# Kernel optimization log

Measured on AMD Instinct MI355X. Metric: run time of the kernel, lower is better.

Reference implementation:

```python
import jax, jax.numpy as jnp
import numpy as np

D_MODEL = 768
N_HEADS = 12
HEAD_DIM = D_MODEL // N_HEADS


def setup_inputs() -> dict:
    key = jax.random.key(0)
    k_x, k_wqkv, k_bqkv, k_wo, k_bo = jax.random.split(key, 5)
    s = 1.0 / np.sqrt(D_MODEL)
    return {
        "x": jax.random.normal(k_x, (4, 2048, D_MODEL), dtype=jnp.float32),
        "W_qkv": jax.random.uniform(k_wqkv, (D_MODEL, 3 * D_MODEL), jnp.float32, -s, s),
        "b_qkv": jax.random.uniform(k_bqkv, (3 * D_MODEL,), jnp.float32, -s, s),
        "W_out": jax.random.uniform(k_wo, (D_MODEL, D_MODEL), jnp.float32, -s, s),
        "b_out": jax.random.uniform(k_bo, (D_MODEL,), jnp.float32, -s, s),
    }


def reference(x, W_qkv, b_qkv, W_out, b_out):
    B, S, D = x.shape
    qkv = x @ W_qkv + b_qkv  # [B, S, 3D]
    q, k, v = jnp.split(qkv, 3, axis=-1)

    def heads(t):
        return t.reshape(B, S, N_HEADS, HEAD_DIM).transpose(0, 2, 1, 3)  # [B,H,S,Dh]

    q, k, v = heads(q), heads(k), heads(v)
    scale = HEAD_DIM ** -0.5
    scores = jnp.einsum("bhqd,bhkd->bhqk", q, k) * scale  # [B,H,S,S]
    causal = jnp.tril(jnp.ones((S, S), dtype=bool))
    scores = jnp.where(causal, scores, -jnp.inf)
    probs = jax.nn.softmax(scores, axis=-1)
    out = jnp.einsum("bhqk,bhkd->bhqd", probs, v)  # [B,H,S,Dh]
    out = out.transpose(0, 2, 1, 3).reshape(B, S, D)
    return out @ W_out + b_out
```

## Files before the change

### kernel.cpp

```cpp
#include <hip/hip_runtime.h>
#include <hip/hip_bf16.h>

#define D_MODEL 768
#define NH 12
#define HD 64
#define BATCH 4
#define SEQ 2048
#define BHN (BATCH*NH)
#define MROWS (BATCH*SEQ)

typedef unsigned short u16;
typedef unsigned int u32;
typedef __attribute__((ext_vector_type(8))) short short8;
typedef __attribute__((ext_vector_type(4))) float f32x4;

__device__ inline u16 f2bf(float f){
  union { __hip_bfloat16 h; u16 u; } cv; cv.h = __float2bfloat16(f); return cv.u;
}
__device__ inline u32 pack_bf2(float a, float b){
  return (u32)f2bf(a) | ((u32)f2bf(b) << 16);
}

__device__ inline void async_copy16(const void* g, void* l){
  __builtin_amdgcn_global_load_lds(
      (const __attribute__((address_space(1))) void*)g,
      (__attribute__((address_space(3))) void*)l, 16, 0, 0);
}

__global__ void cast4_kernel(const float* __restrict__ in, u16* __restrict__ out, int n4){
  int i = blockIdx.x*blockDim.x + threadIdx.x;
  if (i < n4){
    const float4 v = ((const float4*)in)[i];
    ushort4 o;
    o.x = f2bf(v.x); o.y = f2bf(v.y); o.z = f2bf(v.z); o.w = f2bf(v.w);
    ((ushort4*)out)[i] = o;
  }
}

__global__ void transpose_cast_kernel(const float* __restrict__ w, u16* __restrict__ wt,
                                      int K, int N){
  __shared__ u16 tile[64][65];
  int k0 = blockIdx.x*64, n0 = blockIdx.y*64;
  int c = threadIdx.x & 63, r0 = threadIdx.x >> 6;
  #pragma unroll
  for (int r = r0; r < 64; r += 4)
    tile[c][r] = f2bf(w[(size_t)(k0+r)*N + n0 + c]);
  __syncthreads();
  #pragma unroll
  for (int r = r0; r < 64; r += 4)
    wt[(size_t)(n0+r)*K + k0 + c] = tile[r][c];
}

template<int EPI>
__launch_bounds__(256)
__global__ void gemm_bf16(const u16* __restrict__ A, const u16* __restrict__ Bt,
                          const float* __restrict__ bias, float* __restrict__ outf,
                          u16* __restrict__ oq, u16* __restrict__ ok, u16* __restrict__ ovt,
                          int M, int N, int K)
{
  __shared__ alignas(16) char smem[49152];
  const int tid = threadIdx.x, wave = tid>>6, lane = tid&63;
  const int lr = lane&15, lg = lane>>4;
  const int m0 = blockIdx.x*128, n0 = blockIdx.y*128;
  const int wr = (wave>>1)*64, wc = (wave&1)*64;
  f32x4 acc[4][4] = {};
  const int srow = wave*32 + (lane>>2);
  const int schk = (lane&3) ^ ((lane>>3)&3);
  const int fo   = ((lg ^ ((lr>>1)&3)) << 4);

  auto stage = [&](int kt, int buf){
    char* Ab = smem + buf*16384;
    char* Bb = Ab + 8192;
    #pragma unroll
    for (int i = 0; i < 2; i++){
      int r = srow + i*16;
      async_copy16(A  + (size_t)(m0 + r)*K + kt + schk*8, Ab + (wave*32 + i*16)*64);
      async_copy16(Bt + (size_t)(n0 + r)*K + kt + schk*8, Bb + (wave*32 + i*16)*64);
    }
  };

  const int NT = K >> 5;
  stage(0, 0);
  if (NT > 1) stage(32, 1);
  int c = 0, sb = 2;
  for (int t = 0; t < NT; t++){
    if (t+1 < NT) asm volatile("s_waitcnt vmcnt(4)" ::: "memory");
    else          asm volatile("s_waitcnt vmcnt(0)" ::: "memory");
    __builtin_amdgcn_s_barrier();
    if (t+2 < NT){
      stage((t+2)<<5, sb);
      sb = (sb==2) ? 0 : sb+1;
    }

    const char* Ac = smem + c*16384;
    const char* Bc = Ac + 8192;
    c = (c==2) ? 0 : c+1;
    short8 a[4], b[4];
    #pragma unroll
    for (int mi = 0; mi < 4; mi++)
      a[mi] = *(const short8*)(Ac + (wr + mi*16 + lr)*64 + fo);
    #pragma unroll
    for (int ni = 0; ni < 4; ni++)
      b[ni] = *(const short8*)(Bc + (wc + ni*16 + lr)*64 + fo);
    #pragma unroll
    for (int mi = 0; mi < 4; mi++)
      #pragma unroll
      for (int ni = 0; ni < 4; ni++)
        acc[mi][ni] = __builtin_amdgcn_mfma_f32_16x16x32_bf16(a[mi], b[ni], acc[mi][ni], 0, 0, 0);
  }

  #pragma unroll
  for (int mi = 0; mi < 4; mi++)
  #pragma unroll
  for (int ni = 0; ni < 4; ni++)
  #pragma unroll
  for (int j = 0; j < 4; j++){
    int m = m0 + wr + mi*16 + lg*4 + j;
    int n = n0 + wc + ni*16 + lr;
    float v = acc[mi][ni][j] + bias[n];
    if (EPI == 0){
      outf[(size_t)m*N + n] = v;
    } else {
      int b_ = m >> 11, s = m & 2047;
      int t  = (n >= 1536) ? 2 : (n >= 768 ? 1 : 0);
      int hn = n - t*768;
      int h = hn >> 6, d = hn & 63;
      size_t base = (size_t)(b_*NH + h);
      if (t == 0)      oq [(base*SEQ + s)*HD + d] = f2bf(v * 0.1803368801f);
      else if (t == 1) ok [(base*SEQ + s)*HD + d] = f2bf(v);
      else             ovt[(base*HD + d)*SEQ + s] = f2bf(v);
    }
  }
}

__launch_bounds__(256, 3)
__global__ void attn_kernel(const u16* __restrict__ q, const u16* __restrict__ k,
                            const u16* __restrict__ vt, u16* __restrict__ aout)
{
  __shared__ alignas(16) char smem[53248];

  const int b1 = blockIdx.x;
  const int xcd = b1 & 7, grp = b1 >> 3;
  const int bh = xcd*6 + (grp >> 4);
  const int p  = grp & 15;
  const int hi = 31 - p;
  const int tid = threadIdx.x, wave = tid>>6, lane = tid&63;
  const int lr = lane&15, lg = lane>>4;
  const int b_ = bh / NH, h_ = bh % NH;
  const u16* qp = q  + (size_t)bh*SEQ*HD;
  const u16* kp = k  + (size_t)bh*SEQ*HD;
  const u16* vp = vt + (size_t)bh*HD*SEQ;
  char* Pw = smem + 32768 + wave*5120;
  const int fswz = (lr&7)<<4;
  const int c8s = (lane&7) ^ (lane>>3);
  const int nkv = hi + 1;

  auto stageKV = [&](int kv0, int buf){
    char* Kb = smem + buf*16384;
    char* Vb = Kb + 8192;
    #pragma unroll
    for (int r = 0; r < 2; r++){
      int row = wave*16 + r*8 + (lane>>3);
      async_copy16(kp + (size_t)(kv0 + row)*HD + c8s*8, Kb + (wave*16 + r*8)*128);
      async_copy16(vp + (size_t)row*SEQ + kv0 + c8s*8,  Vb + (wave*16 + r*8)*128);
    }
  };

  const int qrow[2] = { hi*64 + wave*16 + lr, p*64 + wave*16 + lr };

  short8 bq[2][2];
  #pragma unroll
  for (int h = 0; h < 2; h++)
    #pragma unroll
    for (int ks = 0; ks < 2; ks++)
      bq[h][ks] = *(const short8*)(qp + (size_t)qrow[h]*HD + ks*32 + lg*8);

  float mrow[2] = {-INFINITY, -INFINITY};
  float lsum[2] = {0.f, 0.f};
  f32x4 o[4][2] = {};

  stageKV(0, 0);

  auto softmax_pack = [&](f32x4 (&s)[4][2], int h, bool domask, int kv0, int qr){
    if (domask){
      #pragma unroll
      for (int ni = 0; ni < 4; ni++)
        #pragma unroll
        for (int jj = 0; jj < 4; jj++){
          int col = kv0 + ni*16 + lg*4 + jj;
          if (col > qr) s[ni][h][jj] = -1e30f;
        }
    }
    float v0 = fmaxf(fmaxf(s[0][h][0], s[0][h][1]), fmaxf(s[0][h][2], s[0][h][3]));
    float v1 = fmaxf(fmaxf(s[1][h][0], s[1][h][1]), fmaxf(s[1][h][2], s[1][h][3]));
    float v2 = fmaxf(fmaxf(s[2][h][0], s[2][h][1]), fmaxf(s[2][h][2], s[2][h][3]));
    float v3 = fmaxf(fmaxf(s[3][h][0], s[3][h][1]), fmaxf(s[3][h][2], s[3][h][3]));
    float vloc = fmaxf(fmaxf(v0, v1), fmaxf(v2, v3));
    if (!__all(vloc - mrow[h] <= 8.0f)){
      float v = fmaxf(vloc, __shfl_xor(vloc, 16));
      v = fmaxf(v, __shfl_xor(v, 32));
      float mn = fmaxf(mrow[h], v);
      float alpha = __builtin_amdgcn_exp2f(mrow[h] - mn);
      mrow[h] = mn;
      lsum[h] *= alpha;
      #pragma unroll
      for (int ni = 0; ni < 4; ni++)
        #pragma unroll
        for (int jj = 0; jj < 4; jj++)
          o[ni][h][jj] *= alpha;
    }
    const float mn = mrow[h];
    char* hb = Pw + h*2560;
    float psum = 0.f;
    #pragma unroll
    for (int ni = 0; ni < 4; ni++){
      float p0 = __builtin_amdgcn_exp2f(s[ni][h][0] - mn);
      float p1 = __builtin_amdgcn_exp2f(s[ni][h][1] - mn);
      float p2 = __builtin_amdgcn_exp2f(s[ni][h][2] - mn);
      float p3 = __builtin_amdgcn_exp2f(s[ni][h][3] - mn);
      psum += (p0+p1) + (p2+p3);
      int tl = lr + 16*(((ni&1)<<1) | (lg>>1));
      int wb = ((ni>>1)<<2) | ((lg&1)<<1);
      *(u32*)(hb + tl*40 + wb*4)     = pack_bf2(p0, p1);
      *(u32*)(hb + tl*40 + wb*4 + 4) = pack_bf2(p2, p3);
    }
    lsum[h] += psum;
  };

  auto read_pb = [&](int h, short8& r0, short8& r1){
    const char* hb = Pw + h*2560 + (size_t)lane*40;
    union { u32 w[4]; short8 v; } a, b;
    a.w[0] = *(const u32*)(hb);      a.w[1] = *(const u32*)(hb + 4);
    a.w[2] = *(const u32*)(hb + 8);  a.w[3] = *(const u32*)(hb + 12);
    b.w[0] = *(const u32*)(hb + 16); b.w[1] = *(const u32*)(hb + 20);
    b.w[2] = *(const u32*)(hb + 24); b.w[3] = *(const u32*)(hb + 28);
    r0 = a.v; r1 = b.v;
  };

  int kvb = 0;

  #pragma unroll 1
  for (; kvb <= p; kvb++){
    const int c = kvb & 1;
    const int kv0 = kvb*64;
    asm volatile("s_waitcnt vmcnt(0)" ::: "memory");
    __builtin_amdgcn_s_barrier();
    if (kvb+1 < nkv) stageKV(kv0 + 64, c^1);

    const char* Kb = smem + c*16384;
    const char* Vb = Kb + 8192;

    f32x4 s[4][2] = {};
    __builtin_amdgcn_s_setprio(1);
    #pragma unroll
    for (int ni = 0; ni < 4; ni++){
      short8 k0 = *(const short8*)(Kb + (ni*16+lr)*128 + ((lg*16) ^ fswz));
      short8 k1 = *(const short8*)(Kb + (ni*16+lr)*128 + ((64 + lg*16) ^ fswz));
      #pragma unroll
      for (int h = 0; h < 2; h++){
        s[ni][h] = __builtin_amdgcn_mfma_f32_16x16x32_bf16(k0, bq[h][0], s[ni][h], 0,0,0);
        s[ni][h] = __builtin_amdgcn_mfma_f32_16x16x32_bf16(k1, bq[h][1], s[ni][h], 0,0,0);
      }
    }
    __builtin_amdgcn_s_setprio(0);

    softmax_pack(s, 0, false, kv0, qrow[0]);
    softmax_pack(s, 1, kvb == p, kv0, qrow[1]);

    short8 pb[2][2];
    read_pb(0, pb[0][0], pb[0][1]);
    read_pb(1, pb[1][0], pb[1][1]);

    __builtin_amdgcn_s_setprio(1);
    #pragma unroll
    for (int ni = 0; ni < 4; ni++){
      short8 v0 = *(const short8*)(Vb + (ni*16+lr)*128 + ((lg*16) ^ fswz));
      short8 v1 = *(const short8*)(Vb + (ni*16+lr)*128 + ((64 + lg*16) ^ fswz));
      #pragma unroll
      for (int h = 0; h < 2; h++){
        o[ni][h] = __builtin_amdgcn_mfma_f32_16x16x32_bf16(v0, pb[h][0], o[ni][h], 0,0,0);
        o[ni][h] = __builtin_amdgcn_mfma_f32_16x16x32_bf16(v1, pb[h][1], o[ni][h], 0,0,0);
      }
    }
    __builtin_amdgcn_s_setprio(0);
  }

  #pragma unroll 1
  for (; kvb < nkv; kvb++){
    const int c = kvb & 1;
    const int kv0 = kvb*64;
    asm volatile("s_waitcnt vmcnt(0)" ::: "memory");
    __builtin_amdgcn_s_barrier();
    if (kvb+1 < nkv) stageKV(kv0 + 64, c^1);

    const char* Kb = smem + c*16384;
    const char* Vb = Kb + 8192;

    f32x4 s[4][2];
    #pragma unroll
    for (int ni = 0; ni < 4; ni++) s[ni][0] = (f32x4){0.f,0.f,0.f,0.f};
    __builtin_amdgcn_s_setprio(1);
    #pragma unroll
    for (int ni = 0; ni < 4; ni++){
      short8 k0 = *(const short8*)(Kb + (ni*16+lr)*128 + ((lg*16) ^ fswz));
      short8 k1 = *(const short8*)(Kb + (ni*16+lr)*128 + ((64 + lg*16) ^ fswz));
      s[ni][0] = __builtin_amdgcn_mfma_f32_16x16x32_bf16(k0, bq[0][0], s[ni][0], 0,0,0);
      s[ni][0] = __builtin_amdgcn_mfma_f32_16x16x32_bf16(k1, bq[0][1], s[ni][0], 0,0,0);
    }
    __builtin_amdgcn_s_setprio(0);

    softmax_pack(s, 0, kvb == hi, kv0, qrow[0]);

    short8 pb0, pb1;
    read_pb(0, pb0, pb1);

    __builtin_amdgcn_s_setprio(1);
    #pragma unroll
    for (int ni = 0; ni < 4; ni++){
      short8 v0 = *(const short8*)(Vb + (ni*16+lr)*128 + ((lg*16) ^ fswz));
      short8 v1 = *(const short8*)(Vb + (ni*16+lr)*128 + ((64 + lg*16) ^ fswz));
      o[ni][0] = __builtin_amdgcn_mfma_f32_16x16x32_bf16(v0, pb0, o[ni][0], 0,0,0);
      o[ni][0] = __builtin_amdgcn_mfma_f32_16x16x32_bf16(v1, pb1, o[ni][0], 0,0,0);
    }
    __builtin_amdgcn_s_setprio(0);
  }

  #pragma unroll
  for (int h = 0; h < 2; h++){
    float ls = lsum[h];
    ls += __shfl_xor(ls, 16);
    ls += __shfl_xor(ls, 32);
    float inv = 1.0f / ls;
    u16* orow = aout + ((size_t)b_*SEQ + qrow[h])*D_MODEL + h_*HD;
    #pragma unroll
    for (int ni = 0; ni < 4; ni++){
      ushort4 w;
      w.x = f2bf(o[ni][h][0]*inv);
      w.y = f2bf(o[ni][h][1]*inv);
      w.z = f2bf(o[ni][h][2]*inv);
      w.w = f2bf(o[ni][h][3]*inv);
      *(ushort4*)(orow + ni*16 + lg*4) = w;
    }
  }
}

extern "C" void kernel_launch(void* const* d_in, const int* in_sizes, int n_in,
                              void* d_out, int out_size, void* d_ws, size_t ws_size,
                              hipStream_t stream)
{
  const float* x    = (const float*)d_in[0];
  const float* Wqkv = (const float*)d_in[1];
  const float* bqkv = (const float*)d_in[2];
  const float* Wout = (const float*)d_in[3];
  const float* bout = (const float*)d_in[4];
  float* out = (float*)d_out;
  char* ws = (char*)d_ws;

  u16* x_bf   = (u16*)(ws + 0);
  u16* wqkv_t = (u16*)(ws + 12582912);
  u16* wout_t = (u16*)(ws + 16121856);
  u16* qb     = (u16*)(ws + 17301504);
  u16* kb     = (u16*)(ws + 29884416);
  u16* vtb    = (u16*)(ws + 42467328);
  u16* attnb  = (u16*)(ws + 55050240);

  cast4_kernel<<<6144, 256, 0, stream>>>(x, x_bf, (BATCH*SEQ*D_MODEL)/4);
  transpose_cast_kernel<<<dim3(12, 36), 256, 0, stream>>>(Wqkv, wqkv_t, 768, 2304);
  transpose_cast_kernel<<<dim3(12, 12), 256, 0, stream>>>(Wout, wout_t, 768, 768);

  gemm_bf16<1><<<dim3(64, 18), 256, 0, stream>>>(x_bf, wqkv_t, bqkv, nullptr,
                                                 qb, kb, vtb, MROWS, 3*D_MODEL, D_MODEL);

  attn_kernel<<<768, 256, 0, stream>>>(qb, kb, vtb, attnb);

  gemm_bf16<0><<<dim3(64, 6), 256, 0, stream>>>(attnb, wout_t, bout, out,
                                                nullptr, nullptr, nullptr, MROWS, D_MODEL, D_MODEL);
}
```

Measured before the change: 139.8 us.

## Replace QKV projection GEMM with 256x256-tile 8-wave pipelined kernel

Adds a dedicated QKV projection kernel that uses 256x256 output tiles, 512 threads and 128KB of dynamic LDS. It double-buffers A and B through async global-to-LDS copies, interleaved with four MFMA phases per K-step, and raises wave priority around the MFMA blocks. The goal is more data reuse per tile and better overlap of loads with matrix math than the old 128x128 GEMM. The cost is 288 blocks spread over the GPU's CUs, which may leave some idle, plus higher register and LDS pressure. The generic GEMM keeps only the plain fp32 epilogue for the output projection.

```diff
diff --git a/kernel.cpp b/kernel.cpp
--- a/kernel.cpp
+++ b/kernel.cpp
@@ -51,11 +51,166 @@
     wt[(size_t)(n0+r)*K + k0 + c] = tile[r][c];
 }
 
+__launch_bounds__(512, 2)
+__global__ void gemm256_qkv(const u16* __restrict__ A, const u16* __restrict__ Bt,
+                            const float* __restrict__ bias,
+                            u16* __restrict__ oq, u16* __restrict__ ok, u16* __restrict__ ovt,
+                            int M, int N, int K)
+{
+  extern __shared__ char smem[];
+  const int tid = threadIdx.x, wid = tid>>6, lane = tid&63;
+  const int wm = wid>>2, wn = wid&3;
+  const int lr = lane&15, lg = lane>>4;
+  const int swz = ((int)blockIdx.x & 7)*36 + ((int)blockIdx.x >> 3);
+  const int m0 = (swz & 31) * 256;
+  const int n0 = (swz >> 5) * 256;
+  const int c8s = (lane&7) ^ (lane>>3);
+  const int srowb = wid*16 + (lane>>3);
+
+  f32x4 acc[8][4] = {};
+
+  auto stageA = [&](int kt, int buf, int half){
+    char* dst = smem + buf*65536 + half*16384 + (wid*16)*128;
+    const u16* src = A + (size_t)(m0 + half*128 + srowb)*K + kt + c8s*8;
+    async_copy16(src,                dst);
+    async_copy16(src + (size_t)8*K,  dst + 1024);
+  };
+  auto stageB = [&](int kt, int buf, int half){
+    char* dst = smem + buf*65536 + 32768 + half*16384 + (wid*16)*128;
+    const u16* src = Bt + (size_t)(n0 + half*128 + srowb)*K + kt + c8s*8;
+    async_copy16(src,                dst);
+    async_copy16(src + (size_t)8*K,  dst + 1024);
+  };
+
+  const int NT = K >> 6;
+  stageA(0, 0, 0); stageA(0, 0, 1); stageB(0, 0, 0); stageB(0, 0, 1);
+  stageB(64, 1, 0); stageB(64, 1, 1);
+  asm volatile("s_waitcnt vmcnt(4)" ::: "memory");
+  __builtin_amdgcn_sched_barrier(0);
+  __builtin_amdgcn_s_barrier();
+
+  short8 a2[4][2], b2[4][2];
+
+  #pragma unroll 1
+  for (int t = 0; t < NT; t++){
+    const int c = t & 1, o = c ^ 1;
+    const char* Ab = smem + c*65536;
+    const char* Bb = Ab + 32768;
+    const int kt1 = (t+1) << 6, kt2 = (t+2) << 6;
+
+    #pragma unroll
+    for (int mi = 0; mi < 4; mi++){
+      int r = wm*128 + mi*16 + lr;
+      a2[mi][0] = *(const short8*)(Ab + r*128 + (( 0 + lg*16) ^ ((r&7)<<4)));
+      a2[mi][1] = *(const short8*)(Ab + r*128 + ((64 + lg*16) ^ ((r&7)<<4)));
+    }
+    #pragma unroll
+    for (int ni = 0; ni < 2; ni++){
+      int r = wn*64 + ni*16 + lr;
+      b2[ni][0] = *(const short8*)(Bb + r*128 + (( 0 + lg*16) ^ ((r&7)<<4)));
+      b2[ni][1] = *(const short8*)(Bb + r*128 + ((64 + lg*16) ^ ((r&7)<<4)));
+    }
+    if (t+1 < NT) stageA(kt1, o, 0);
+    __builtin_amdgcn_s_barrier();
+    asm volatile("s_waitcnt lgkmcnt(0)" ::: "memory");
+    __builtin_amdgcn_sched_barrier(0);
+    __builtin_amdgcn_s_setprio(1);
+    #pragma unroll
+    for (int mi = 0; mi < 4; mi++)
+      #pragma unroll
+      for (int ni = 0; ni < 2; ni++){
+        acc[mi][ni] = __builtin_amdgcn_mfma_f32_16x16x32_bf16(a2[mi][0], b2[ni][0], acc[mi][ni], 0,0,0);
+        acc[mi][ni] = __builtin_amdgcn_mfma_f32_16x16x32_bf16(a2[mi][1], b2[ni][1], acc[mi][ni], 0,0,0);
+      }
+    __builtin_amdgcn_s_setprio(0);
+    __builtin_amdgcn_s_barrier();
+
+    #pragma unroll
+    for (int ni = 2; ni < 4; ni++){
+      int r = wn*64 + ni*16 + lr;
+      b2[ni][0] = *(const short8*)(Bb + r*128 + (( 0 + lg*16) ^ ((r&7)<<4)));
+      b2[ni][1] = *(const short8*)(Bb + r*128 + ((64 + lg*16) ^ ((r&7)<<4)));
+    }
+    if (t+1 < NT) stageA(kt1, o, 1);
+    __builtin_amdgcn_s_barrier();
+    asm volatile("s_waitcnt lgkmcnt(0)" ::: "memory");
+    __builtin_amdgcn_sched_barrier(0);
+    __builtin_amdgcn_s_setprio(1);
+    #pragma unroll
+    for (int mi = 0; mi < 4; mi++)
+      #pragma unroll
+      for (int ni = 2; ni < 4; ni++){
+        acc[mi][ni] = __builtin_amdgcn_mfma_f32_16x16x32_bf16(a2[mi][0], b2[ni][0], acc[mi][ni], 0,0,0);
+        acc[mi][ni] = __builtin_amdgcn_mfma_f32_16x16x32_bf16(a2[mi][1], b2[ni][1], acc[mi][ni], 0,0,0);
+      }
+    __builtin_amdgcn_s_setprio(0);
+    __builtin_amdgcn_s_barrier();
+
+    #pragma unroll
+    for (int mi = 0; mi < 4; mi++){
+      int r = wm*128 + (mi+4)*16 + lr;
+      a2[mi][0] = *(const short8*)(Ab + r*128 + (( 0 + lg*16) ^ ((r&7)<<4)));
+      a2[mi][1] = *(const short8*)(Ab + r*128 + ((64 + lg*16) ^ ((r&7)<<4)));
+    }
+    if (t+2 < NT) stageB(kt2, c, 0);
+    __builtin_amdgcn_s_barrier();
+    asm volatile("s_waitcnt lgkmcnt(0)" ::: "memory");
+    __builtin_amdgcn_sched_barrier(0);
+    __builtin_amdgcn_s_setprio(1);
+    #pragma unroll
+    for (int mi = 0; mi < 4; mi++)
+      #pragma unroll
+      for (int ni = 0; ni < 2; ni++){
+        acc[4+mi][ni] = __builtin_amdgcn_mfma_f32_16x16x32_bf16(a2[mi][0], b2[ni][0], acc[4+mi][ni], 0,0,0);
+        acc[4+mi][ni] = __builtin_amdgcn_mfma_f32_16x16x32_bf16(a2[mi][1], b2[ni][1], acc[4+mi][ni], 0,0,0);
+      }
+    __builtin_amdgcn_s_setprio(0);
+    __builtin_amdgcn_s_barrier();
+
+    if (t+2 < NT){
+      asm volatile("s_waitcnt vmcnt(2)" ::: "memory");
+    } else {
+      asm volatile("s_waitcnt vmcnt(0)" ::: "memory");
+    }
+    __builtin_amdgcn_sched_barrier(0);
+    if (t+2 < NT) stageB(kt2, c, 1);
+    __builtin_amdgcn_s_barrier();
+    __builtin_amdgcn_s_setprio(1);
+    #pragma unroll
+    for (int mi = 0; mi < 4; mi++)
+      #pragma unroll
+      for (int ni = 2; ni < 4; ni++){
+        acc[4+mi][ni] = __builtin_amdgcn_mfma_f32_16x16x32_bf16(a2[mi][0], b2[ni][0], acc[4+mi][ni], 0,0,0);
+        acc[4+mi][ni] = __builtin_amdgcn_mfma_f32_16x16x32_bf16(a2[mi][1], b2[ni][1], acc[4+mi][ni], 0,0,0);
+      }
+    __builtin_amdgcn_s_setprio(0);
+    __builtin_amdgcn_s_barrier();
+  }
+
+  #pragma unroll
+  for (int mi = 0; mi < 8; mi++)
+  #pragma unroll
+  for (int ni = 0; ni < 4; ni++)
+  #pragma unroll
+  for (int j = 0; j < 4; j++){
+    int m = m0 + wm*128 + mi*16 + lg*4 + j;
+    int n = n0 + wn*64 + ni*16 + lr;
+    float v = acc[mi][ni][j] + bias[n];
+    int b_ = m >> 11, s = m & 2047;
+    int ty = (n >= 1536) ? 2 : (n >= 768 ? 1 : 0);
+    int hn = n - ty*768;
+    int h = hn >> 6, d = hn & 63;
+    size_t base = (size_t)(b_*NH + h);
+    if (ty == 0)      oq [(base*SEQ + s)*HD + d] = f2bf(v * 0.1803368801f);
+    else if (ty == 1) ok [(base*SEQ + s)*HD + d] = f2bf(v);
+    else              ovt[(base*HD + d)*SEQ + s] = f2bf(v);
+  }
+}
+
 template<int EPI>
 __launch_bounds__(256)
 __global__ void gemm_bf16(const u16* __restrict__ A, const u16* __restrict__ Bt,
                           const float* __restrict__ bias, float* __restrict__ outf,
-                          u16* __restrict__ oq, u16* __restrict__ ok, u16* __restrict__ ovt,
                           int M, int N, int K)
 {
   __shared__ alignas(16) char smem[49152];
@@ -117,19 +272,7 @@
   for (int j = 0; j < 4; j++){
     int m = m0 + wr + mi*16 + lg*4 + j;
     int n = n0 + wc + ni*16 + lr;
-    float v = acc[mi][ni][j] + bias[n];
-    if (EPI == 0){
-      outf[(size_t)m*N + n] = v;
-    } else {
-      int b_ = m >> 11, s = m & 2047;
-      int t  = (n >= 1536) ? 2 : (n >= 768 ? 1 : 0);
-      int hn = n - t*768;
-      int h = hn >> 6, d = hn & 63;
-      size_t base = (size_t)(b_*NH + h);
-      if (t == 0)      oq [(base*SEQ + s)*HD + d] = f2bf(v * 0.1803368801f);
-      else if (t == 1) ok [(base*SEQ + s)*HD + d] = f2bf(v);
-      else             ovt[(base*HD + d)*SEQ + s] = f2bf(v);
-    }
+    outf[(size_t)m*N + n] = acc[mi][ni][j] + bias[n];
   }
 }
 
@@ -138,7 +281,6 @@
                             const u16* __restrict__ vt, u16* __restrict__ aout)
 {
   __shared__ alignas(16) char smem[53248];
-
   const int b1 = blockIdx.x;
   const int xcd = b1 & 7, grp = b1 >> 3;
   const int bh = xcd*6 + (grp >> 4);
@@ -364,15 +506,18 @@
   u16* vtb    = (u16*)(ws + 42467328);
   u16* attnb  = (u16*)(ws + 55050240);
 
+  hipFuncSetAttribute((const void*)gemm256_qkv,
+                      hipFuncAttributeMaxDynamicSharedMemorySize, 131072);
+
   cast4_kernel<<<6144, 256, 0, stream>>>(x, x_bf, (BATCH*SEQ*D_MODEL)/4);
   transpose_cast_kernel<<<dim3(12, 36), 256, 0, stream>>>(Wqkv, wqkv_t, 768, 2304);
   transpose_cast_kernel<<<dim3(12, 12), 256, 0, stream>>>(Wout, wout_t, 768, 768);
 
-  gemm_bf16<1><<<dim3(64, 18), 256, 0, stream>>>(x_bf, wqkv_t, bqkv, nullptr,
-                                                 qb, kb, vtb, MROWS, 3*D_MODEL, D_MODEL);
+  gemm256_qkv<<<288, 512, 131072, stream>>>(x_bf, wqkv_t, bqkv,
+                                            qb, kb, vtb, MROWS, 3*D_MODEL, D_MODEL);
 
   attn_kernel<<<768, 256, 0, stream>>>(qb, kb, vtb, attnb);
 
   gemm_bf16<0><<<dim3(64, 6), 256, 0, stream>>>(attnb, wout_t, bout, out,
-                                                nullptr, nullptr, nullptr, MROWS, D_MODEL, D_MODEL);
-}
+                                                MROWS, D_MODEL, D_MODEL);
+}
```

Measured after the change: 184.6 us. 1.32x slower.
